# Kernel optimization log

Measured on AMD Instinct MI355X. Metric: run time of the kernel, lower is better.

The kernel has to match this reference:

```python
import jax, jax.numpy as jnp
import numpy as np

D = 1024

def setup_inputs() -> dict:
    key = jax.random.key(0)
    ks = jax.random.split(key, 7)
    s = 1.0 / np.sqrt(D)
    x = jax.random.normal(ks[0], (4, 4096, D), dtype=jnp.float32)
    Wi = jax.random.uniform(ks[1], (2 * D, D), jnp.float32, -s, s)   # in_proj weight [2D, D]
    bi = jax.random.uniform(ks[2], (2 * D,), jnp.float32, -s, s)
    Wc = jax.random.uniform(ks[3], (D, 1, 3), jnp.float32, -0.577, 0.577)  # depthwise conv [D,1,3]
    bc = jax.random.uniform(ks[4], (D,), jnp.float32, -0.577, 0.577)
    Wo = jax.random.uniform(ks[5], (D, D), jnp.float32, -s, s)       # out_proj weight [D, D]
    bo = jax.random.uniform(ks[6], (D,), jnp.float32, -s, s)
    return {"x": x, "Wi": Wi, "bi": bi, "Wc": Wc, "bc": bc, "Wo": Wo, "bo": bo}

def _depthwise_conv1d(v, Wc, bc):
    # v: [B, L, D] -> NCH [B, D, L]; kernel [D, 1, 3] (OIH), groups = D; pad 1 both sides
    y = jax.lax.conv_general_dilated(
        v.transpose(0, 2, 1), Wc,
        window_strides=(1,), padding=[(1, 1)],
        dimension_numbers=("NCH", "OIH", "NCH"),
        feature_group_count=v.shape[-1])
    return y.transpose(0, 2, 1) + bc  # [B, L, D]

def reference(x, Wi, bi, Wc, bc, Wo, bo):
    uv = jnp.einsum("bld,ed->ble", x, Wi) + bi        # [B, L, 2D]
    u, v = jnp.split(uv, 2, axis=-1)                   # each [B, L, D]
    y = _depthwise_conv1d(v, Wc, bc)
    y = jax.nn.silu(y) * u                             # fused gate
    return jnp.einsum("bld,ed->ble", y, Wo) + bo       # [B, L, D]
```

## Files before the change

### kernel.cpp

```cpp
#include <hip/hip_runtime.h>
#include <math.h>


typedef __attribute__((ext_vector_type(8))) short short8;
typedef __attribute__((ext_vector_type(4))) float floatx4;

__device__ __forceinline__ float b2f(short s) {
    unsigned int u = ((unsigned int)(unsigned short)s) << 16;
    float f;
    __builtin_memcpy(&f, &u, 4);
    return f;
}

__device__ __forceinline__ short f2b(float f) {
    unsigned int u;
    __builtin_memcpy(&u, &f, 4);
    u += 0x7fffu + ((u >> 16) & 1u);
    return (short)(u >> 16);
}

__device__ __forceinline__ void gl_lds16(const short* g, short* l) {
    __builtin_amdgcn_global_load_lds(
        (const __attribute__((address_space(1))) unsigned int*)g,
        (__attribute__((address_space(3))) unsigned int*)l,
        16, 0, 0);
}

__global__ __launch_bounds__(256) void cvt_all(
    const float* __restrict__ x, const float* __restrict__ Wi,
    const float* __restrict__ Wo, short* __restrict__ xb,
    short* __restrict__ Wib, short* __restrict__ Wob)
{
    constexpr int n1 = 16384 * 1024 / 8;
    constexpr int n2 = 2048 * 1024 / 8;
    constexpr int n3 = 1024 * 1024 / 8;
    int i = blockIdx.x * 256 + threadIdx.x;
    const float* src;
    short* dst;
    int j;
    if (i < n1)           { src = x;  dst = xb;  j = i; }
    else if (i < n1 + n2) { src = Wi; dst = Wib; j = i - n1; }
    else if (i < n1 + n2 + n3) { src = Wo; dst = Wob; j = i - n1 - n2; }
    else return;
    float4 a = ((const float4*)src)[2 * j];
    float4 b = ((const float4*)src)[2 * j + 1];
    short8 o;
    o[0] = f2b(a.x); o[1] = f2b(a.y); o[2] = f2b(a.z); o[3] = f2b(a.w);
    o[4] = f2b(b.x); o[5] = f2b(b.y); o[6] = f2b(b.z); o[7] = f2b(b.w);
    ((short8*)dst)[j] = o;
}

#define GB_TILE(SLOT, WAIT, ST)                                              \
  {                                                                          \
    asm volatile(WAIT ::: "memory");                                         \
    __builtin_amdgcn_s_barrier();                                            \
    asm volatile("" ::: "memory");                                           \
    if ((ST) >= 0) {                                                         \
        gl_lds16(gA + (size_t)(ST) * 32, lA0 + ((ST) & 3) * 8192);           \
        gl_lds16(gA + (size_t)(ST) * 32 + (size_t)16 * lda,                  \
                 lA0 + ((ST) & 3) * 8192 + 512);                             \
    }                                                                        \
    const short* Ab = &As[(SLOT) * 8192];                                    \
    const short* Bb = &Bs[(SLOT) * 8192];                                    \
    short8 av0[4], av1[4], bvv[4];                                           \
    _Pragma("unroll") for (int ni = 0; ni < 4; ni++)                         \
        bvv[ni] = *(const short8*)&Bb[bBase + ni * 512];                     \
    _Pragma("unroll") for (int mi = 0; mi < 4; mi++)                         \
        av0[mi] = *(const short8*)&Ab[aBase + mi * 512];                     \
    asm volatile("s_waitcnt lgkmcnt(0)" ::: "memory");                       \
    __builtin_amdgcn_sched_barrier(0);                                       \
    __builtin_amdgcn_s_setprio(1);                                           \
    _Pragma("unroll") for (int mi = 0; mi < 4; mi++)                         \
      _Pragma("unroll") for (int ni = 0; ni < 4; ni++)                       \
        acc[mi][ni] = __builtin_amdgcn_mfma_f32_16x16x32_bf16(               \
            av0[mi], bvv[ni], acc[mi][ni], 0, 0, 0);                         \
    __builtin_amdgcn_s_setprio(0);                                           \
    __builtin_amdgcn_s_barrier();                                            \
    asm volatile("" ::: "memory");                                           \
    if ((ST) >= 0) {                                                         \
        gl_lds16(gB + (size_t)(ST) * 32, lB0 + ((ST) & 3) * 8192);           \
        gl_lds16(gB + (size_t)(ST) * 32 + (size_t)16 * ldb,                  \
                 lB0 + ((ST) & 3) * 8192 + 512);                             \
    }                                                                        \
    _Pragma("unroll") for (int mi = 0; mi < 4; mi++)                         \
        av1[mi] = *(const short8*)&Ab[aBase + (4 + mi) * 512];               \
    asm volatile("s_waitcnt lgkmcnt(0)" ::: "memory");                       \
    __builtin_amdgcn_sched_barrier(0);                                       \
    __builtin_amdgcn_s_setprio(1);                                           \
    _Pragma("unroll") for (int mi = 0; mi < 4; mi++)                         \
      _Pragma("unroll") for (int ni = 0; ni < 4; ni++)                       \
        acc[4 + mi][ni] = __builtin_amdgcn_mfma_f32_16x16x32_bf16(           \
            av1[mi], bvv[ni], acc[4 + mi][ni], 0, 0, 0);                     \
    __builtin_amdgcn_s_setprio(0);                                           \
  }

template <bool OUTF32>
__global__ __launch_bounds__(512, 2) void gemm_bt(
    const short* __restrict__ A, const short* __restrict__ B,
    const float* __restrict__ bias, void* __restrict__ Cv,
    int lda, int ldb, int ldc)
{
    __shared__ __attribute__((aligned(16))) short As[4 * 8192];
    __shared__ __attribute__((aligned(16))) short Bs[4 * 8192];

    const int tid  = threadIdx.x;
    const int wave = tid >> 6;
    const int lane = tid & 63;

    const int nwg = gridDim.x * gridDim.y;
    const int f   = blockIdx.y * gridDim.x + blockIdx.x;
    const int nf  = (f & 7) * (nwg >> 3) + (f >> 3);
    const int mBase = (nf / gridDim.x) * 256;
    const int nBase = (nf % gridDim.x) * 256;

    floatx4 acc[8][4];
#pragma unroll
    for (int i = 0; i < 8; i++)
#pragma unroll
        for (int j = 0; j < 4; j++) acc[i][j] = {0.f, 0.f, 0.f, 0.f};

    const int srow = lane >> 2;
    const int sg   = ((lane & 3) ^ ((srow >> 1) & 3)) * 8;
    const short* gA = A + (size_t)(mBase + wave * 32 + srow) * lda + sg;
    const short* gB = B + (size_t)(nBase + wave * 32 + srow) * ldb + sg;
    short* lA0 = &As[wave * 1024];
    short* lB0 = &Bs[wave * 1024];

    const int fRow = lane & 15;
    const int lg   = lane >> 4;
    const int pg8  = (lg ^ ((fRow >> 1) & 3)) * 8;
    const int mq   = (wave >> 2) * 128;
    const int nq   = (wave & 3) * 64;
    const int aBase = (mq + fRow) * 32 + pg8;
    const int bBase = (nq + fRow) * 32 + pg8;

#pragma unroll
    for (int p = 0; p < 3; p++) {
        gl_lds16(gA + (size_t)p * 32, lA0 + p * 8192);
        gl_lds16(gA + (size_t)p * 32 + (size_t)16 * lda, lA0 + p * 8192 + 512);
        gl_lds16(gB + (size_t)p * 32, lB0 + p * 8192);
        gl_lds16(gB + (size_t)p * 32 + (size_t)16 * ldb, lB0 + p * 8192 + 512);
    }

    for (int tb = 0; tb < 28; tb += 4) {
        GB_TILE(0, "s_waitcnt vmcnt(8)", tb + 3)
        GB_TILE(1, "s_waitcnt vmcnt(8)", tb + 4)
        GB_TILE(2, "s_waitcnt vmcnt(8)", tb + 5)
        GB_TILE(3, "s_waitcnt vmcnt(8)", tb + 6)
    }
    GB_TILE(0, "s_waitcnt vmcnt(8)", 31)
    GB_TILE(1, "s_waitcnt vmcnt(8)", -1)
    GB_TILE(2, "s_waitcnt vmcnt(4)", -1)
    GB_TILE(3, "s_waitcnt vmcnt(0)", -1)

    const int colq = lane & 15;
    const int rowq = lg * 4;
#pragma unroll
    for (int ni = 0; ni < 4; ni++) {
        const int col = nBase + nq + ni * 16 + colq;
        const float bvv2 = bias[col];
#pragma unroll
        for (int mi = 0; mi < 8; mi++) {
            const int row = mBase + mq + mi * 16 + rowq;
#pragma unroll
            for (int r = 0; r < 4; r++) {
                float v = acc[mi][ni][r] + bvv2;
                if (OUTF32)
                    ((float*)Cv)[(size_t)(row + r) * ldc + col] = v;
                else
                    ((short*)Cv)[(size_t)(row + r) * ldc + col] = f2b(v);
            }
        }
    }
}

__global__ __launch_bounds__(256) void conv_gate(
    const short* __restrict__ uv, const float* __restrict__ Wc,
    const float* __restrict__ bc, short* __restrict__ yb)
{
    const int idx = blockIdx.x * 256 + threadIdx.x;
    const int d8 = idx & 127;
    const int m  = idx >> 7;
    const int l  = m & 4095;
    const int d  = d8 * 8;

    float w[24];
#pragma unroll
    for (int q = 0; q < 6; q++)
        *(float4*)&w[q * 4] = ((const float4*)(Wc + d * 3))[q];
    float bcv[8];
    *(float4*)&bcv[0] = ((const float4*)(bc + d))[0];
    *(float4*)&bcv[4] = ((const float4*)(bc + d))[1];

    const size_t rowu = (size_t)m * 2048 + d;
    const size_t rowv = rowu + 1024;

    const short8 z = {0, 0, 0, 0, 0, 0, 0, 0};
    const short8 us = *(const short8*)(uv + rowu);
    const short8 vc = *(const short8*)(uv + rowv);
    const short8 vm = (l > 0)    ? *(const short8*)(uv + rowv - 2048) : z;
    const short8 vp = (l < 4095) ? *(const short8*)(uv + rowv + 2048) : z;

    short8 outv;
#pragma unroll
    for (int j = 0; j < 8; j++) {
        float y = b2f(vm[j]) * w[j * 3 + 0]
                + b2f(vc[j]) * w[j * 3 + 1]
                + b2f(vp[j]) * w[j * 3 + 2]
                + bcv[j];
        float sil = y / (1.0f + expf(-y));
        outv[j] = f2b(sil * b2f(us[j]));
    }
    *(short8*)(yb + (size_t)m * 1024 + d) = outv;
}

extern "C" void kernel_launch(void* const* d_in, const int* in_sizes, int n_in,
                              void* d_out, int out_size, void* d_ws, size_t ws_size,
                              hipStream_t stream)
{
    const float* x  = (const float*)d_in[0];
    const float* Wi = (const float*)d_in[1];
    const float* bi = (const float*)d_in[2];
    const float* Wc = (const float*)d_in[3];
    const float* bc = (const float*)d_in[4];
    const float* Wo = (const float*)d_in[5];
    const float* bo = (const float*)d_in[6];
    float* out = (float*)d_out;

    short* wsS = (short*)d_ws;
    short* uv  = wsS;
    short* xb  = uv + (size_t)16384 * 2048;
    short* Wib = xb + (size_t)16384 * 1024;
    short* Wob = Wib + (size_t)2048 * 1024;

    dim3 blk(256);
    dim3 blkG(512);

    constexpr int nCvt = (16384 * 1024 + 2048 * 1024 + 1024 * 1024) / 8;
    cvt_all<<<(nCvt + 255) / 256, blk, 0, stream>>>(x, Wi, Wo, xb, Wib, Wob);

    dim3 g1(2048 / 256, 16384 / 256);
    gemm_bt<false><<<g1, blkG, 0, stream>>>(xb, Wib, bi, uv, 1024, 1024, 2048);

    conv_gate<<<(16384 * 128) / 256, blk, 0, stream>>>(uv, Wc, bc, xb);

    dim3 g2(1024 / 256, 16384 / 256);
    gemm_bt<true><<<g2, blkG, 0, stream>>>(xb, Wob, bo, out, 1024, 1024, 1024);
}
```

Measured before the change: 288.2 us.

## Double-buffer LDS fragments in registers and drop one barrier per k-tile

Result: slower. 299.5 us (+3.9%).

```diff
diff --git a/kernel.cpp b/kernel.cpp
--- a/kernel.cpp
+++ b/kernel.cpp
@@ -50,48 +50,42 @@
     ((short8*)dst)[j] = o;
 }
 
-#define GB_TILE(SLOT, WAIT, ST)                                              \
-  {                                                                          \
-    asm volatile(WAIT ::: "memory");                                         \
-    __builtin_amdgcn_s_barrier();                                            \
-    asm volatile("" ::: "memory");                                           \
-    if ((ST) >= 0) {                                                         \
-        gl_lds16(gA + (size_t)(ST) * 32, lA0 + ((ST) & 3) * 8192);           \
-        gl_lds16(gA + (size_t)(ST) * 32 + (size_t)16 * lda,                  \
-                 lA0 + ((ST) & 3) * 8192 + 512);                             \
-    }                                                                        \
-    const short* Ab = &As[(SLOT) * 8192];                                    \
-    const short* Bb = &Bs[(SLOT) * 8192];                                    \
-    short8 av0[4], av1[4], bvv[4];                                           \
-    _Pragma("unroll") for (int ni = 0; ni < 4; ni++)                         \
-        bvv[ni] = *(const short8*)&Bb[bBase + ni * 512];                     \
-    _Pragma("unroll") for (int mi = 0; mi < 4; mi++)                         \
-        av0[mi] = *(const short8*)&Ab[aBase + mi * 512];                     \
-    asm volatile("s_waitcnt lgkmcnt(0)" ::: "memory");                       \
-    __builtin_amdgcn_sched_barrier(0);                                       \
-    __builtin_amdgcn_s_setprio(1);                                           \
-    _Pragma("unroll") for (int mi = 0; mi < 4; mi++)                         \
-      _Pragma("unroll") for (int ni = 0; ni < 4; ni++)                       \
-        acc[mi][ni] = __builtin_amdgcn_mfma_f32_16x16x32_bf16(               \
-            av0[mi], bvv[ni], acc[mi][ni], 0, 0, 0);                         \
-    __builtin_amdgcn_s_setprio(0);                                           \
-    __builtin_amdgcn_s_barrier();                                            \
-    asm volatile("" ::: "memory");                                           \
-    if ((ST) >= 0) {                                                         \
-        gl_lds16(gB + (size_t)(ST) * 32, lB0 + ((ST) & 3) * 8192);           \
-        gl_lds16(gB + (size_t)(ST) * 32 + (size_t)16 * ldb,                  \
-                 lB0 + ((ST) & 3) * 8192 + 512);                             \
-    }                                                                        \
-    _Pragma("unroll") for (int mi = 0; mi < 4; mi++)                         \
-        av1[mi] = *(const short8*)&Ab[aBase + (4 + mi) * 512];               \
-    asm volatile("s_waitcnt lgkmcnt(0)" ::: "memory");                       \
-    __builtin_amdgcn_sched_barrier(0);                                       \
-    __builtin_amdgcn_s_setprio(1);                                           \
-    _Pragma("unroll") for (int mi = 0; mi < 4; mi++)                         \
-      _Pragma("unroll") for (int ni = 0; ni < 4; ni++)                       \
-        acc[4 + mi][ni] = __builtin_amdgcn_mfma_f32_16x16x32_bf16(           \
-            av1[mi], bvv[ni], acc[4 + mi][ni], 0, 0, 0);                     \
-    __builtin_amdgcn_s_setprio(0);                                           \
+#define GB_TILE(SLOT, NSLOT, P, NP, WAIT, ST, PREF)                           \
+  {                                                                           \
+    asm volatile(WAIT ::: "memory");                                          \
+    __builtin_amdgcn_s_barrier();                                             \
+    asm volatile("" ::: "memory");                                            \
+    if ((ST) >= 0) {                                                          \
+        gl_lds16(gA + (size_t)(ST) * 32, lA0 + ((ST) & 3) * 8192);            \
+        gl_lds16(gA + (size_t)(ST) * 32 + (size_t)16 * lda,                   \
+                 lA0 + ((ST) & 3) * 8192 + 512);                              \
+    }                                                                         \
+    short8 a1_[4];                                                            \
+    _Pragma("unroll") for (int mi = 0; mi < 4; mi++)                          \
+        a1_[mi] = *(const short8*)&As[(SLOT) * 8192 + aBase + (4 + mi) * 512];\
+    __builtin_amdgcn_s_setprio(1);                                            \
+    _Pragma("unroll") for (int mi = 0; mi < 4; mi++)                          \
+      _Pragma("unroll") for (int ni = 0; ni < 4; ni++)                        \
+        acc[mi][ni] = __builtin_amdgcn_mfma_f32_16x16x32_bf16(                \
+            a0[P][mi], bvv[P][ni], acc[mi][ni], 0, 0, 0);                     \
+    __builtin_amdgcn_s_setprio(0);                                            \
+    if ((ST) >= 0) {                                                          \
+        gl_lds16(gB + (size_t)(ST) * 32, lB0 + ((ST) & 3) * 8192);            \
+        gl_lds16(gB + (size_t)(ST) * 32 + (size_t)16 * ldb,                   \
+                 lB0 + ((ST) & 3) * 8192 + 512);                              \
+    }                                                                         \
+    if (PREF) {                                                               \
+      _Pragma("unroll") for (int ni = 0; ni < 4; ni++)                        \
+        bvv[NP][ni] = *(const short8*)&Bs[(NSLOT) * 8192 + bBase + ni * 512]; \
+      _Pragma("unroll") for (int mi = 0; mi < 4; mi++)                        \
+        a0[NP][mi] = *(const short8*)&As[(NSLOT) * 8192 + aBase + mi * 512];  \
+    }                                                                         \
+    __builtin_amdgcn_s_setprio(1);                                            \
+    _Pragma("unroll") for (int mi = 0; mi < 4; mi++)                          \
+      _Pragma("unroll") for (int ni = 0; ni < 4; ni++)                        \
+        acc[4 + mi][ni] = __builtin_amdgcn_mfma_f32_16x16x32_bf16(            \
+            a1_[mi], bvv[P][ni], acc[4 + mi][ni], 0, 0, 0);                   \
+    __builtin_amdgcn_s_setprio(0);                                            \
   }
 
 template <bool OUTF32>
@@ -134,6 +128,8 @@
     const int aBase = (mq + fRow) * 32 + pg8;
     const int bBase = (nq + fRow) * 32 + pg8;
 
+    short8 bvv[2][4], a0[2][4];
+
 #pragma unroll
     for (int p = 0; p < 3; p++) {
         gl_lds16(gA + (size_t)p * 32, lA0 + p * 8192);
@@ -141,30 +137,39 @@
         gl_lds16(gB + (size_t)p * 32, lB0 + p * 8192);
         gl_lds16(gB + (size_t)p * 32 + (size_t)16 * ldb, lB0 + p * 8192 + 512);
     }
+    asm volatile("s_waitcnt vmcnt(8)" ::: "memory");
+    __builtin_amdgcn_s_barrier();
+    asm volatile("" ::: "memory");
+#pragma unroll
+    for (int ni = 0; ni < 4; ni++)
+        bvv[0][ni] = *(const short8*)&Bs[bBase + ni * 512];
+#pragma unroll
+    for (int mi = 0; mi < 4; mi++)
+        a0[0][mi] = *(const short8*)&As[aBase + mi * 512];
 
     for (int tb = 0; tb < 28; tb += 4) {
-        GB_TILE(0, "s_waitcnt vmcnt(8)", tb + 3)
-        GB_TILE(1, "s_waitcnt vmcnt(8)", tb + 4)
-        GB_TILE(2, "s_waitcnt vmcnt(8)", tb + 5)
-        GB_TILE(3, "s_waitcnt vmcnt(8)", tb + 6)
-    }
-    GB_TILE(0, "s_waitcnt vmcnt(8)", 31)
-    GB_TILE(1, "s_waitcnt vmcnt(8)", -1)
-    GB_TILE(2, "s_waitcnt vmcnt(4)", -1)
-    GB_TILE(3, "s_waitcnt vmcnt(0)", -1)
+        GB_TILE(0, 1, 0, 1, "s_waitcnt vmcnt(4)", tb + 3, 1)
+        GB_TILE(1, 2, 1, 0, "s_waitcnt vmcnt(4)", tb + 4, 1)
+        GB_TILE(2, 3, 0, 1, "s_waitcnt vmcnt(4)", tb + 5, 1)
+        GB_TILE(3, 0, 1, 0, "s_waitcnt vmcnt(4)", tb + 6, 1)
+    }
+    GB_TILE(0, 1, 0, 1, "s_waitcnt vmcnt(4)", 31, 1)
+    GB_TILE(1, 2, 1, 0, "s_waitcnt vmcnt(4)", -1, 1)
+    GB_TILE(2, 3, 0, 1, "s_waitcnt vmcnt(0)", -1, 1)
+    GB_TILE(3, 0, 1, 0, "s_waitcnt vmcnt(0)", -1, 0)
 
     const int colq = lane & 15;
     const int rowq = lg * 4;
 #pragma unroll
     for (int ni = 0; ni < 4; ni++) {
         const int col = nBase + nq + ni * 16 + colq;
-        const float bvv2 = bias[col];
+        const float bsv = bias[col];
 #pragma unroll
         for (int mi = 0; mi < 8; mi++) {
             const int row = mBase + mq + mi * 16 + rowq;
 #pragma unroll
             for (int r = 0; r < 4; r++) {
-                float v = acc[mi][ni][r] + bvv2;
+                float v = acc[mi][ni][r] + bsv;
                 if (OUTF32)
                     ((float*)Cv)[(size_t)(row + r) * ldc + col] = v;
                 else
```
